# Kernel tuning notes

Hardware: AMD Instinct MI355X
Metric: run time of the kernel (lower is better)

## Reference

```python
import jax, jax.numpy as jnp
import numpy as np

B, C_IN, C_OUT, K, H, W_DIM, F_IN = 16, 64, 64, 3, 128, 128, 16
NKW = C_OUT * C_IN * K * K  # 36864 kernel weights per sample


def setup_inputs() -> dict:
    key = jax.random.key(0)
    ks = jax.random.split(key, 8)
    s = 0.05
    return {
        "x": jax.random.normal(ks[0], (B, C_IN, H, W_DIM), dtype=jnp.float32),
        "z": jax.random.normal(ks[1], (B, F_IN), dtype=jnp.float32),
        "W0": jax.random.normal(ks[2], (20, F_IN), dtype=jnp.float32) * s,
        "b0": jax.random.normal(ks[3], (20,), dtype=jnp.float32) * s,
        "W1": jax.random.normal(ks[4], (30, 20), dtype=jnp.float32) * s,
        "b1": jax.random.normal(ks[5], (30,), dtype=jnp.float32) * s,
        "W2": jax.random.normal(ks[6], (NKW + C_OUT, 30), dtype=jnp.float32) * s,
        "b2": jax.random.normal(ks[7], (NKW + C_OUT,), dtype=jnp.float32) * s,
    }


def reference(x, z, W0, b0, W1, b1, W2, b2):
    # Manifold MLP: ReLU after EVERY layer, including the final one (as in original code).
    h = jax.nn.relu(z @ W0.T + b0)
    h = jax.nn.relu(h @ W1.T + b1)
    aw = jax.nn.relu(h @ W2.T + b2)  # [B, NKW + C_OUT]

    kernels = aw[:, :NKW].reshape(B, C_OUT, C_IN, K, K)  # per-sample OIHW kernels
    biases = aw[:, NKW:]  # [B, C_OUT]

    def conv_one(xi, wi, bi):
        # xi: [C_IN, H, W], wi: [C_OUT, C_IN, K, K], bi: [C_OUT]
        y = jax.lax.conv_general_dilated(
            xi[None], wi, window_strides=(1, 1), padding="SAME",
            dimension_numbers=("NCHW", "OIHW", "NCHW"))[0]
        return y + bi[:, None, None]

    out = jax.vmap(conv_one)(x, kernels, biases)  # [B, C_OUT, H, W]
    return jax.nn.relu(out)
```

## Files before the change

### kernel.cpp

```cpp
#include <hip/hip_runtime.h>


typedef __bf16 bf16;
typedef __bf16 bf16x8 __attribute__((ext_vector_type(8)));
typedef float f32x4 __attribute__((ext_vector_type(4)));

#define NB 16
#define CI 64
#define CO 64
#define HH 128
#define WW 128
#define TS 16
#define HALO 18
#define NPL (HALO * HALO)
#define NKW 36864
#define NROWS 36928
#define WT2_BYTES ((size_t)NB * 9 * 4096 * 2)

__global__ __launch_bounds__(256)
void hyper_kernel(const float* __restrict__ z, const float* __restrict__ W0,
                  const float* __restrict__ b0, const float* __restrict__ W1,
                  const float* __restrict__ b1, const float* __restrict__ W2,
                  const float* __restrict__ b2, bf16* __restrict__ wt2,
                  float* __restrict__ biases) {
  __shared__ float h1s[NB][30];
  const int tid = threadIdx.x;
  if (tid < NB) {
    float h0[20];
    #pragma unroll
    for (int i = 0; i < 20; ++i) {
      float s = b0[i];
      #pragma unroll
      for (int j = 0; j < 16; ++j) s += W0[i * 16 + j] * z[tid * 16 + j];
      h0[i] = fmaxf(s, 0.f);
    }
    #pragma unroll
    for (int i = 0; i < 30; ++i) {
      float s = b1[i];
      #pragma unroll
      for (int j = 0; j < 20; ++j) s += W1[i * 20 + j] * h0[j];
      h1s[tid][i] = fmaxf(s, 0.f);
    }
  }
  __syncthreads();
  const int r = blockIdx.x * 256 + tid;
  if (r >= NROWS) return;
  float w2r[30];
  #pragma unroll
  for (int j = 0; j < 30; ++j) w2r[j] = W2[r * 30 + j];
  const float bb = b2[r];
  const bool isk = r < NKW;
  size_t base = 0;
  if (isk) {
    const int co = r / 576;
    const int rem = r - co * 576;
    const int ci = rem / 9;
    const int tap = rem - ci * 9;
    const int g = co >> 4, mm = co & 15;
    const int kh = ci >> 5, qq = (ci >> 3) & 3, jj = ci & 7;
    base = (size_t)(tap * 8 + g * 2 + kh) * 512 + (size_t)(qq * 16 + mm) * 8 + jj;
  }
  for (int b = 0; b < NB; ++b) {
    float s = bb;
    #pragma unroll
    for (int j = 0; j < 30; ++j) s += w2r[j] * h1s[b][j];
    s = fmaxf(s, 0.f);
    if (isk)
      wt2[(size_t)b * (9 * 4096) + base] = (bf16)s;
    else
      biases[b * CO + (r - NKW)] = s;
  }
}

__global__ __launch_bounds__(512, 4)
void conv_kernel(const float* __restrict__ x, const bf16* __restrict__ wt2,
                 const float* __restrict__ bias, float* __restrict__ out) {
  __shared__ __align__(16) bf16 xt[NPL * 64];

  const int id = (blockIdx.x & 7) * 128 + (blockIdx.x >> 3);
  const int b = id >> 6;
  const int x0 = (id & 7) * TS;
  const int y0 = ((id >> 3) & 7) * TS;

  const int tid = threadIdx.x;
  const int lane = tid & 63;
  const int wv = tid >> 6;
  const int m = lane & 15;
  const int q = lane >> 4;

  const char* wbase = (const char*)wt2 + (size_t)b * (9 * 8192) + lane * 16;

  bf16x8 abuf[2][4][2];
  #pragma unroll
  for (int i = 0; i < 4; ++i)
    #pragma unroll
    for (int kh = 0; kh < 2; ++kh)
      abuf[0][i][kh] =
          *reinterpret_cast<const bf16x8*>(wbase + (i * 2 + kh) * 1024);

  const float* xb = x + ((size_t)b << 20);
  float vbuf[6][8];
  int pls[6], cigs[6];
  bool inbs[6];
  #pragma unroll
  for (int t = 0; t < 6; ++t) {
    const int it = min(tid + t * 512, NPL * 8 - 1);
    const int cig = ((it >> 2) * 810) >> 16;
    const int pl = it - cig * 324;
    const int py = (pl * 57) >> 10;
    const int px = pl - py * 18;
    int gy = y0 + py - 1, gx = x0 + px - 1;
    inbs[t] = ((unsigned)gy < (unsigned)HH) & ((unsigned)gx < (unsigned)WW);
    gy = min(max(gy, 0), HH - 1);
    gx = min(max(gx, 0), WW - 1);
    pls[t] = pl;
    cigs[t] = cig;
    const float* src = xb + ((size_t)cig << 17) + (gy << 7) + gx;
    #pragma unroll
    for (int j = 0; j < 8; ++j) vbuf[t][j] = src[(size_t)j << 14];
  }

  #pragma unroll
  for (int t = 0; t < 6; ++t) {
    if (t == 5 && tid >= NPL * 8 - 5 * 512) break;
    bf16x8 v8;
    #pragma unroll
    for (int j = 0; j < 8; ++j)
      v8[j] = inbs[t] ? (bf16)vbuf[t][j] : (bf16)0.f;
    *reinterpret_cast<bf16x8*>(reinterpret_cast<char*>(xt) + (pls[t] << 7) +
                               ((cigs[t] ^ (pls[t] & 7)) << 4)) = v8;
  }

  f32x4 acc[4][2];
  #pragma unroll
  for (int i = 0; i < 4; ++i) {
    acc[i][0] = (f32x4){0.f, 0.f, 0.f, 0.f};
    acc[i][1] = (f32x4){0.f, 0.f, 0.f, 0.f};
  }

  const int ty0 = wv * 2;

  __syncthreads();

  #pragma unroll
  for (int tap = 0; tap < 9; ++tap) {
    const int cur = tap & 1, nxt = cur ^ 1;
    if (tap < 8) {
      const char* wt_n = wbase + (tap + 1) * 8192;
      #pragma unroll
      for (int i = 0; i < 4; ++i)
        #pragma unroll
        for (int kh = 0; kh < 2; ++kh)
          abuf[nxt][i][kh] =
              *reinterpret_cast<const bf16x8*>(wt_n + (i * 2 + kh) * 1024);
    }
    const int dy = (tap * 11) >> 5;
    const int dx = tap - dy * 3;
    const int plb = (ty0 + dy) * 18 + dx + m;
    __builtin_amdgcn_s_setprio(1);
    #pragma unroll
    for (int kh = 0; kh < 2; ++kh) {
      const int qk = q + kh * 4;
      #pragma unroll
      for (int j = 0; j < 2; ++j) {
        const int pl = plb + j * 18;
        const bf16x8 bv = *reinterpret_cast<const bf16x8*>(
            reinterpret_cast<const char*>(xt) + (pl << 7) +
            ((qk ^ (pl & 7)) << 4));
        #pragma unroll
        for (int i = 0; i < 4; ++i)
          acc[i][j] = __builtin_amdgcn_mfma_f32_16x16x32_bf16(
              abuf[cur][i][kh], bv, acc[i][j], 0, 0, 0);
      }
    }
    __builtin_amdgcn_s_setprio(0);
  }

  const float* bp = bias + b * CO;
  float* ob = out + ((size_t)(b * CO) << 14) + (size_t)((y0 + ty0) * WW + x0 + m);
  #pragma unroll
  for (int i = 0; i < 4; ++i)
    #pragma unroll
    for (int j = 0; j < 2; ++j)
      #pragma unroll
      for (int r = 0; r < 4; ++r) {
        const int co = i * 16 + q * 4 + r;
        float v = acc[i][j][r] + bp[co];
        ob[((size_t)co << 14) + j * WW] = fmaxf(v, 0.f);
      }
}

extern "C" void kernel_launch(void* const* d_in, const int* in_sizes, int n_in,
                              void* d_out, int out_size, void* d_ws,
                              size_t ws_size, hipStream_t stream) {
  const float* x = (const float*)d_in[0];
  const float* z = (const float*)d_in[1];
  const float* W0 = (const float*)d_in[2];
  const float* b0 = (const float*)d_in[3];
  const float* W1 = (const float*)d_in[4];
  const float* b1 = (const float*)d_in[5];
  const float* W2 = (const float*)d_in[6];
  const float* b2 = (const float*)d_in[7];
  float* out = (float*)d_out;

  bf16* wt2 = (bf16*)d_ws;
  float* biases = (float*)((char*)d_ws + WT2_BYTES);

  hipLaunchKernelGGL(hyper_kernel, dim3((NROWS + 255) / 256), dim3(256), 0,
                     stream, z, W0, b0, W1, b1, W2, b2, wt2, biases);
  hipLaunchKernelGGL(conv_kernel, dim3(1024), dim3(512), 0, stream, x, wt2,
                     biases, out);
}
```

Baseline: 179.4 us.

## Pre-pack input into padded NHWC bf16 and stage weights in LDS

The prep kernel now also converts x into a zero-padded 130x130 channels-last bf16 buffer in workspace, using extra blocks alongside the hypernetwork rows. The conv kernel then reads input fragments straight from global memory (relying on cache for halo reuse) and stages the per-sample weights into LDS via global_load_lds. This is meant to remove the strided fp32 gather, the conversion and the halo-tile LDS build from every conv block. In exchange it adds a full extra write and read of the converted input, and a fallback keeps the old path when the workspace is too small.

```diff
diff --git a/kernel.cpp b/kernel.cpp
--- a/kernel.cpp
+++ b/kernel.cpp
@@ -15,67 +15,108 @@
 #define NPL (HALO * HALO)
 #define NKW 36864
 #define NROWS 36928
+#define XHW 130
 #define WT2_BYTES ((size_t)NB * 9 * 4096 * 2)
+#define BIAS_BYTES 4096
+#define XH_BYTES ((size_t)NB * XHW * XHW * CI * 2)
+#define WS_NEED (WT2_BYTES + BIAS_BYTES + XH_BYTES)
+
+typedef const __attribute__((address_space(1))) void* gas_ptr;
+typedef __attribute__((address_space(3))) void* las_ptr;
 
 __global__ __launch_bounds__(256)
-void hyper_kernel(const float* __restrict__ z, const float* __restrict__ W0,
-                  const float* __restrict__ b0, const float* __restrict__ W1,
-                  const float* __restrict__ b1, const float* __restrict__ W2,
-                  const float* __restrict__ b2, bf16* __restrict__ wt2,
-                  float* __restrict__ biases) {
-  __shared__ float h1s[NB][30];
+void prep_kernel(const float* __restrict__ x, const float* __restrict__ z,
+                 const float* __restrict__ W0, const float* __restrict__ b0,
+                 const float* __restrict__ W1, const float* __restrict__ b1,
+                 const float* __restrict__ W2, const float* __restrict__ b2,
+                 bf16* __restrict__ wt2, float* __restrict__ biases,
+                 bf16* __restrict__ xh) {
   const int tid = threadIdx.x;
-  if (tid < NB) {
-    float h0[20];
-    #pragma unroll
-    for (int i = 0; i < 20; ++i) {
-      float s = b0[i];
-      #pragma unroll
-      for (int j = 0; j < 16; ++j) s += W0[i * 16 + j] * z[tid * 16 + j];
-      h0[i] = fmaxf(s, 0.f);
-    }
-    #pragma unroll
-    for (int i = 0; i < 30; ++i) {
-      float s = b1[i];
-      #pragma unroll
-      for (int j = 0; j < 20; ++j) s += W1[i * 20 + j] * h0[j];
-      h1s[tid][i] = fmaxf(s, 0.f);
-    }
-  }
-  __syncthreads();
-  const int r = blockIdx.x * 256 + tid;
-  if (r >= NROWS) return;
-  float w2r[30];
-  #pragma unroll
-  for (int j = 0; j < 30; ++j) w2r[j] = W2[r * 30 + j];
-  const float bb = b2[r];
-  const bool isk = r < NKW;
-  size_t base = 0;
-  if (isk) {
-    const int co = r / 576;
-    const int rem = r - co * 576;
-    const int ci = rem / 9;
-    const int tap = rem - ci * 9;
-    const int g = co >> 4, mm = co & 15;
-    const int kh = ci >> 5, qq = (ci >> 3) & 3, jj = ci & 7;
-    base = (size_t)(tap * 8 + g * 2 + kh) * 512 + (size_t)(qq * 16 + mm) * 8 + jj;
-  }
-  for (int b = 0; b < NB; ++b) {
-    float s = bb;
-    #pragma unroll
-    for (int j = 0; j < 30; ++j) s += w2r[j] * h1s[b][j];
-    s = fmaxf(s, 0.f);
-    if (isk)
-      wt2[(size_t)b * (9 * 4096) + base] = (bf16)s;
-    else
-      biases[b * CO + (r - NKW)] = s;
-  }
+  if (blockIdx.x < 145) {
+    __shared__ float h1s[NB][30];
+    if (tid < NB) {
+      float h0[20];
+      #pragma unroll
+      for (int i = 0; i < 20; ++i) {
+        float s = b0[i];
+        #pragma unroll
+        for (int j = 0; j < 16; ++j) s += W0[i * 16 + j] * z[tid * 16 + j];
+        h0[i] = fmaxf(s, 0.f);
+      }
+      #pragma unroll
+      for (int i = 0; i < 30; ++i) {
+        float s = b1[i];
+        #pragma unroll
+        for (int j = 0; j < 20; ++j) s += W1[i * 20 + j] * h0[j];
+        h1s[tid][i] = fmaxf(s, 0.f);
+      }
+    }
+    __syncthreads();
+    const int r = blockIdx.x * 256 + tid;
+    if (r >= NROWS) return;
+    float w2r[30];
+    #pragma unroll
+    for (int j = 0; j < 30; ++j) w2r[j] = W2[r * 30 + j];
+    const float bb = b2[r];
+    const bool isk = r < NKW;
+    size_t base = 0;
+    if (isk) {
+      const int co = r / 576;
+      const int rem = r - co * 576;
+      const int ci = rem / 9;
+      const int tap = rem - ci * 9;
+      const int g = co >> 4, mm = co & 15;
+      const int kh = ci >> 5, qq = (ci >> 3) & 3, jj = ci & 7;
+      base = (size_t)(tap * 8 + g * 2 + kh) * 512 + (size_t)(qq * 16 + mm) * 8 + jj;
+    }
+    for (int b = 0; b < NB; ++b) {
+      float s = bb;
+      #pragma unroll
+      for (int j = 0; j < 30; ++j) s += w2r[j] * h1s[b][j];
+      s = fmaxf(s, 0.f);
+      if (isk)
+        wt2[(size_t)b * (9 * 4096) + base] = (bf16)s;
+      else
+        biases[b * CO + (r - NKW)] = s;
+    }
+    return;
+  }
+
+  const int bi = blockIdx.x - 145;
+  const int b = bi / XHW;
+  const int yp = bi - b * XHW;
+  bf16* row = xh + ((size_t)(b * XHW + yp)) * XHW * CI;
+  const bf16x8 zero8 = {};
+  if (yp == 0 || yp == XHW - 1) {
+    for (int g = tid; g < XHW * 8; g += 256)
+      *reinterpret_cast<bf16x8*>(row + g * 8) = zero8;
+    return;
+  }
+  if (tid < 8)
+    *reinterpret_cast<bf16x8*>(row + tid * 8) = zero8;
+  else if (tid >= 248)
+    *reinterpret_cast<bf16x8*>(row + (XHW - 1) * CI + (tid - 248) * 8) = zero8;
+
+  const int px = tid & 127;
+  const int c0 = (tid >> 7) * 32;
+  const float* src =
+      x + (((size_t)b * CI + c0) << 14) + ((size_t)(yp - 1) << 7) + px;
+  bf16x8 v[4];
+  #pragma unroll
+  for (int g = 0; g < 4; ++g)
+    #pragma unroll
+    for (int j = 0; j < 8; ++j)
+      v[g][j] = (bf16)src[((size_t)(g * 8 + j)) << 14];
+  bf16* dst = row + (px + 1) * CI + c0;
+  #pragma unroll
+  for (int g = 0; g < 4; ++g)
+    *reinterpret_cast<bf16x8*>(dst + g * 8) = v[g];
 }
 
 __global__ __launch_bounds__(512, 4)
-void conv_kernel(const float* __restrict__ x, const bf16* __restrict__ wt2,
+void conv_kernel(const bf16* __restrict__ xh, const bf16* __restrict__ wt2,
                  const float* __restrict__ bias, float* __restrict__ out) {
-  __shared__ __align__(16) bf16 xt[NPL * 64];
+  __shared__ __align__(16) bf16 wts[9 * 4096];
 
   const int id = (blockIdx.x & 7) * 128 + (blockIdx.x >> 3);
   const int b = id >> 6;
@@ -88,6 +129,100 @@
   const int m = lane & 15;
   const int q = lane >> 4;
 
+  {
+    const bf16* g = wt2 + (size_t)b * (9 * 4096);
+    #pragma unroll
+    for (int k = 0; k < 9; ++k) {
+      const int off = (k * 512 + wv * 64) * 8;
+      __builtin_amdgcn_global_load_lds((gas_ptr)(g + off + lane * 8),
+                                       (las_ptr)(wts + off), 16, 0, 0);
+    }
+  }
+
+  const int ty0 = wv * 2;
+  const bf16* xb = xh + (((size_t)b * XHW + (y0 + ty0)) * XHW + (x0 + m)) * CI +
+                   q * 8;
+  const bf16* rp[4];
+  #pragma unroll
+  for (int r = 0; r < 4; ++r) rp[r] = xb + (size_t)r * XHW * CI;
+
+  f32x4 acc[4][2];
+  #pragma unroll
+  for (int i = 0; i < 4; ++i) {
+    acc[i][0] = (f32x4){0.f, 0.f, 0.f, 0.f};
+    acc[i][1] = (f32x4){0.f, 0.f, 0.f, 0.f};
+  }
+
+  bf16x8 bb[2][2][2];
+  #pragma unroll
+  for (int kh = 0; kh < 2; ++kh)
+    #pragma unroll
+    for (int j = 0; j < 2; ++j)
+      bb[0][kh][j] = *reinterpret_cast<const bf16x8*>(rp[j] + kh * 32);
+
+  __syncthreads();
+
+  #pragma unroll
+  for (int tap = 0; tap < 9; ++tap) {
+    const int cur = tap & 1, nxt = cur ^ 1;
+    if (tap < 8) {
+      const int dyn = (tap + 1) / 3, dxn = (tap + 1) - dyn * 3;
+      #pragma unroll
+      for (int kh = 0; kh < 2; ++kh)
+        #pragma unroll
+        for (int j = 0; j < 2; ++j)
+          bb[nxt][kh][j] = *reinterpret_cast<const bf16x8*>(
+              rp[j + dyn] + dxn * 64 + kh * 32);
+    }
+    bf16x8 a[4][2];
+    #pragma unroll
+    for (int i = 0; i < 4; ++i)
+      #pragma unroll
+      for (int kh = 0; kh < 2; ++kh)
+        a[i][kh] = *reinterpret_cast<const bf16x8*>(
+            wts + tap * 4096 + (i * 2 + kh) * 512 + lane * 8);
+    __builtin_amdgcn_s_setprio(1);
+    #pragma unroll
+    for (int kh = 0; kh < 2; ++kh)
+      #pragma unroll
+      for (int j = 0; j < 2; ++j)
+        #pragma unroll
+        for (int i = 0; i < 4; ++i)
+          acc[i][j] = __builtin_amdgcn_mfma_f32_16x16x32_bf16(
+              a[i][kh], bb[cur][kh][j], acc[i][j], 0, 0, 0);
+    __builtin_amdgcn_s_setprio(0);
+  }
+
+  const float* bp = bias + b * CO;
+  float* ob = out + ((size_t)(b * CO) << 14) + (size_t)((y0 + ty0) * WW + x0 + m);
+  #pragma unroll
+  for (int i = 0; i < 4; ++i)
+    #pragma unroll
+    for (int j = 0; j < 2; ++j)
+      #pragma unroll
+      for (int r = 0; r < 4; ++r) {
+        const int co = i * 16 + q * 4 + r;
+        float v = acc[i][j][r] + bp[co];
+        ob[((size_t)co << 14) + j * WW] = fmaxf(v, 0.f);
+      }
+}
+
+__global__ __launch_bounds__(512, 4)
+void conv_fb(const float* __restrict__ x, const bf16* __restrict__ wt2,
+             const float* __restrict__ bias, float* __restrict__ out) {
+  __shared__ __align__(16) bf16 xt[NPL * 64];
+
+  const int id = (blockIdx.x & 7) * 128 + (blockIdx.x >> 3);
+  const int b = id >> 6;
+  const int x0 = (id & 7) * TS;
+  const int y0 = ((id >> 3) & 7) * TS;
+
+  const int tid = threadIdx.x;
+  const int lane = tid & 63;
+  const int wv = tid >> 6;
+  const int m = lane & 15;
+  const int q = lane >> 4;
+
   const char* wbase = (const char*)wt2 + (size_t)b * (9 * 8192) + lane * 16;
 
   bf16x8 abuf[2][4][2];
@@ -99,10 +234,6 @@
           *reinterpret_cast<const bf16x8*>(wbase + (i * 2 + kh) * 1024);
 
   const float* xb = x + ((size_t)b << 20);
-  float vbuf[6][8];
-  int pls[6], cigs[6];
-  bool inbs[6];
-  #pragma unroll
   for (int t = 0; t < 6; ++t) {
     const int it = min(tid + t * 512, NPL * 8 - 1);
     const int cig = ((it >> 2) * 810) >> 16;
@@ -110,25 +241,17 @@
     const int py = (pl * 57) >> 10;
     const int px = pl - py * 18;
     int gy = y0 + py - 1, gx = x0 + px - 1;
-    inbs[t] = ((unsigned)gy < (unsigned)HH) & ((unsigned)gx < (unsigned)WW);
+    const bool inb = ((unsigned)gy < (unsigned)HH) & ((unsigned)gx < (unsigned)WW);
     gy = min(max(gy, 0), HH - 1);
     gx = min(max(gx, 0), WW - 1);
-    pls[t] = pl;
-    cigs[t] = cig;
     const float* src = xb + ((size_t)cig << 17) + (gy << 7) + gx;
-    #pragma unroll
-    for (int j = 0; j < 8; ++j) vbuf[t][j] = src[(size_t)j << 14];
-  }
-
-  #pragma unroll
-  for (int t = 0; t < 6; ++t) {
-    if (t == 5 && tid >= NPL * 8 - 5 * 512) break;
     bf16x8 v8;
     #pragma unroll
     for (int j = 0; j < 8; ++j)
-      v8[j] = inbs[t] ? (bf16)vbuf[t][j] : (bf16)0.f;
-    *reinterpret_cast<bf16x8*>(reinterpret_cast<char*>(xt) + (pls[t] << 7) +
-                               ((cigs[t] ^ (pls[t] & 7)) << 4)) = v8;
+      v8[j] = inb ? (bf16)src[(size_t)j << 14] : (bf16)0.f;
+    if (!(t == 5 && tid >= NPL * 8 - 5 * 512))
+      *reinterpret_cast<bf16x8*>(reinterpret_cast<char*>(xt) + (pl << 7) +
+                                 ((cig ^ (pl & 7)) << 4)) = v8;
   }
 
   f32x4 acc[4][2];
@@ -137,9 +260,7 @@
     acc[i][0] = (f32x4){0.f, 0.f, 0.f, 0.f};
     acc[i][1] = (f32x4){0.f, 0.f, 0.f, 0.f};
   }
-
   const int ty0 = wv * 2;
-
   __syncthreads();
 
   #pragma unroll
@@ -205,9 +326,17 @@
 
   bf16* wt2 = (bf16*)d_ws;
   float* biases = (float*)((char*)d_ws + WT2_BYTES);
-
-  hipLaunchKernelGGL(hyper_kernel, dim3((NROWS + 255) / 256), dim3(256), 0,
-                     stream, z, W0, b0, W1, b1, W2, b2, wt2, biases);
-  hipLaunchKernelGGL(conv_kernel, dim3(1024), dim3(512), 0, stream, x, wt2,
-                     biases, out);
+  bf16* xh = (bf16*)((char*)d_ws + WT2_BYTES + BIAS_BYTES);
+
+  if (ws_size >= WS_NEED) {
+    hipLaunchKernelGGL(prep_kernel, dim3(145 + NB * XHW), dim3(256), 0, stream,
+                       x, z, W0, b0, W1, b1, W2, b2, wt2, biases, xh);
+    hipLaunchKernelGGL(conv_kernel, dim3(1024), dim3(512), 0, stream, xh, wt2,
+                       biases, out);
+  } else {
+    hipLaunchKernelGGL(prep_kernel, dim3(145), dim3(256), 0, stream, x, z, W0,
+                       b0, W1, b1, W2, b2, wt2, biases, xh);
+    hipLaunchKernelGGL(conv_fb, dim3(1024), dim3(512), 0, stream, x, wt2,
+                       biases, out);
+  }
 }
```

Result: faster. 174.6 us (-2.7%).
